# Kernel optimization log

Hardware: AMD Instinct MI355X
Metric: run time of the kernel (lower is better)

The kernel has to match this reference:

```python
import jax, jax.numpy as jnp
import numpy as np

B, T, D, H, V, NV = 64, 1024, 128, 256, 128, 3


def setup_inputs() -> dict:
    key = jax.random.key(0)
    ks = jax.random.split(key, 8)
    s_ih = 1.0 / np.sqrt(H)
    return {
        "x": jax.random.normal(ks[0], (B, T, D), dtype=jnp.float32),
        # PyTorch LSTM params: gate order i, f, g, o along the 4H axis
        "W_ih": jax.random.uniform(ks[1], (4 * H, D), minval=-s_ih, maxval=s_ih, dtype=jnp.float32),
        "W_hh": jax.random.uniform(ks[2], (4 * H, H), minval=-s_ih, maxval=s_ih, dtype=jnp.float32),
        "b_ih": jax.random.uniform(ks[3], (4 * H,), minval=-s_ih, maxval=s_ih, dtype=jnp.float32),
        "b_hh": jax.random.uniform(ks[4], (4 * H,), minval=-s_ih, maxval=s_ih, dtype=jnp.float32),
        "head_w": jax.random.uniform(ks[5], (NV, V, H), minval=-s_ih, maxval=s_ih, dtype=jnp.float32),
        "head_b": jax.random.uniform(ks[6], (NV, V), minval=-s_ih, maxval=s_ih, dtype=jnp.float32),
    }


def _lstm(x, W_ih, W_hh, b_ih, b_hh):
    Bc, Tc, _ = x.shape
    Hc = W_hh.shape[1]
    # Precompute input contribution for all timesteps in one GEMM: [B,T,4H]
    gx = jnp.einsum('btd,gd->btg', x, W_ih) + b_ih + b_hh
    gx = jnp.transpose(gx, (1, 0, 2))  # [T,B,4H] for scan over time

    def step(carry, g_t):
        h, c = carry
        g = g_t + h @ W_hh.T  # [B,4H]
        i, f, gg, o = jnp.split(g, 4, axis=-1)
        i = jax.nn.sigmoid(i)
        f = jax.nn.sigmoid(f)
        o = jax.nn.sigmoid(o)
        c = f * c + i * jnp.tanh(gg)
        h = o * jnp.tanh(c)
        return (h, c), h

    h0 = jnp.zeros((Bc, Hc), dtype=x.dtype)
    c0 = jnp.zeros((Bc, Hc), dtype=x.dtype)
    _, hs = jax.lax.scan(step, (h0, c0), gx)  # hs: [T,B,H]
    return jnp.transpose(hs, (1, 0, 2))  # [B,T,H]


def reference(x, W_ih, W_hh, b_ih, b_hh, head_w, head_b):
    out = _lstm(x, W_ih, W_hh, b_ih, b_hh)  # [B,T,H]
    # 3 parallel heads fused into one batched GEMM: [NV,B,T,V]
    logits = jnp.einsum('bth,nvh->nbtv', out, head_w) + head_b[:, None, None, :]
    return (logits[0], logits[1], logits[2])
```

## Files before the change

### kernel.cpp

```cpp
#include <hip/hip_runtime.h>
#include <hip/hip_bf16.h>
#include <math.h>

#define Bb 64
#define Tt 1024
#define Dd 128
#define Hh 256
#define G4 1024
#define Vv 128
#define NVh 3
#define BT (Bb*Tt)

typedef __fp16 half2_t __attribute__((ext_vector_type(2)));
typedef __fp16 f16x4 __attribute__((ext_vector_type(4)));
typedef __fp16 f16x8 __attribute__((ext_vector_type(8)));
typedef float f32x4 __attribute__((ext_vector_type(4)));

__device__ __forceinline__ half2_t pkh(float a, float b) {
    return __builtin_amdgcn_cvt_pkrtz(a, b);
}
__device__ __forceinline__ half2_t bch(unsigned int x) {
    return __builtin_bit_cast(half2_t, x);
}
__device__ __forceinline__ unsigned int bcu(half2_t x) {
    return __builtin_bit_cast(unsigned int, x);
}
__device__ __forceinline__ float fsig(float x) {
    return __builtin_amdgcn_rcpf(1.f + __expf(-x));
}
__device__ __forceinline__ float ftanh(float x) {
    float e = __expf(-2.f * fabsf(x));
    float r = (1.f - e) * __builtin_amdgcn_rcpf(1.f + e);
    return copysignf(r, x);
}
__device__ __forceinline__ f16x8 pk8f(const float* p) {
    float4 a = *(const float4*)p;
    float4 b = *(const float4*)(p + 4);
    uint4 u;
    u.x = bcu(pkh(a.x, a.y));
    u.y = bcu(pkh(a.z, a.w));
    u.z = bcu(pkh(b.x, b.y));
    u.w = bcu(pkh(b.z, b.w));
    return __builtin_bit_cast(f16x8, u);
}
__device__ __forceinline__ int sdot4(int a, int b, int c) {
#if __has_builtin(__builtin_amdgcn_sdot4)
    return __builtin_amdgcn_sdot4(a, b, c, false);
#else
    int r = c;
    #pragma unroll
    for (int i = 0; i < 4; ++i) {
        int av = (a << (24 - 8 * i)) >> 24;
        int bv = (b << (24 - 8 * i)) >> 24;
        r += av * bv;
    }
    return r;
#endif
}

__global__ __launch_bounds__(256) void cvt16(const float* __restrict__ in,
                                             __fp16* __restrict__ out, int n4) {
    int i = blockIdx.x * 256 + threadIdx.x;
    if (i < n4) {
        float4 v = ((const float4*)in)[i];
        f16x4 o;
        o[0] = (__fp16)v.x; o[1] = (__fp16)v.y;
        o[2] = (__fp16)v.z; o[3] = (__fp16)v.w;
        ((f16x4*)out)[i] = o;
    }
}

__global__ __launch_bounds__(256) void gx_mfma(const float* __restrict__ x,
                                               const __fp16* __restrict__ Wih16,
                                               const float* __restrict__ bih,
                                               const float* __restrict__ bhh,
                                               __fp16* __restrict__ gx2) {
    const int tid = threadIdx.x;
    const int w = tid >> 6, l = tid & 63;
    const int mb = blockIdx.x * 64 + w * 16;
    const int lr = l & 15, lk = l >> 4;

    f16x8 af[4];
    const float* xa = x + (size_t)(mb + lr) * Dd + lk * 8;
    #pragma unroll
    for (int ks = 0; ks < 4; ++ks) af[ks] = pk8f(xa + ks * 32);

    for (int jt = 0; jt < 16; ++jt) {
        f32x4 acc[4] = {};
        #pragma unroll
        for (int ks = 0; ks < 4; ++ks) {
            #pragma unroll
            for (int g = 0; g < 4; ++g) {
                const __fp16* bb = Wih16 + (size_t)(g * 256 + jt * 16 + lr) * Dd + ks * 32 + lk * 8;
                f16x8 bf = *(const f16x8*)bb;
                acc[g] = __builtin_amdgcn_mfma_f32_16x16x32_f16(af[ks], bf, acc[g], 0, 0, 0);
            }
        }
        float bsum[4];
        #pragma unroll
        for (int g = 0; g < 4; ++g) {
            int j = g * 256 + jt * 16 + lr;
            bsum[g] = bih[j] + bhh[j];
        }
        #pragma unroll
        for (int r = 0; r < 4; ++r) {
            int m = mb + lk * 4 + r;
            f16x4 o;
            o[0] = (__fp16)(acc[0][r] + bsum[0]);
            o[1] = (__fp16)(acc[1][r] + bsum[1]);
            o[2] = (__fp16)(acc[2][r] + bsum[2]);
            o[3] = (__fp16)(acc[3][r] + bsum[3]);
            *(f16x4*)&gx2[((size_t)m * Hh + jt * 16 + lr) * 4] = o;
        }
    }
}

__global__ __launch_bounds__(512, 2) void lstm_scan(const __fp16* __restrict__ gx2,
                                                    const float* __restrict__ Whh,
                                                    __fp16* __restrict__ hs16) {
    __shared__ __align__(16) unsigned int hq[64];
    __shared__ __align__(16) float4 pex[256];
    const int tid = threadIdx.x;
    const int jj = tid & 255;
    const int s = tid >> 8;
    const int b = blockIdx.x;

    int wq[4][32];
    #pragma unroll
    for (int g = 0; g < 4; ++g) {
        const float* wr = Whh + (size_t)(g * 256 + jj) * Hh + s * 128;
        #pragma unroll
        for (int c = 0; c < 32; ++c) {
            float4 f = *(const float4*)&wr[c * 4];
            int q0 = (int)rintf(f.x * 2032.f);
            int q1 = (int)rintf(f.y * 2032.f);
            int q2 = (int)rintf(f.z * 2032.f);
            int q3 = (int)rintf(f.w * 2032.f);
            wq[g][c] = (q0 & 255) | ((q1 & 255) << 8) | ((q2 & 255) << 16) | (q3 << 24);
        }
    }
    if (tid < 64) hq[tid] = 0u;
    float c_state = 0.f;
    __syncthreads();

    const __fp16* gxb = gx2 + ((size_t)b * Tt * Hh + jj) * 4;
    __fp16* hsb = hs16 + (size_t)b * Tt * Hh + jj;

    float g0 = 0.f, g1 = 0.f, g2 = 0.f, g3 = 0.f;
    if (s == 0) {
        uint2 gv = *(const uint2*)gxb;
        half2_t p = bch(gv.x), q = bch(gv.y);
        g0 = (float)p[0]; g1 = (float)p[1]; g2 = (float)q[0]; g3 = (float)q[1];
    }

    const uint4* h16 = (const uint4*)hq + (s << 3);
    __fp16 hprev = (__fp16)0.f;
    const float INV = 1.f / (2032.f * 127.f);

    for (int t = 0; t < Tt; ++t) {
        if (s == 0 && t > 0) hsb[(size_t)(t - 1) * Hh] = hprev;

        float n0 = 0.f, n1 = 0.f, n2 = 0.f, n3 = 0.f;
        if (s == 0) {
            const __fp16* gn = gxb + (size_t)(t + 1 < Tt ? t + 1 : t) * 1024;
            uint2 gv = *(const uint2*)gn;
            half2_t p = bch(gv.x), q = bch(gv.y);
            n0 = (float)p[0]; n1 = (float)p[1]; n2 = (float)q[0]; n3 = (float)q[1];
        }

        int a0 = 0, a1 = 0, a2 = 0, a3 = 0;
        #pragma unroll
        for (int q = 0; q < 8; ++q) {
            uint4 hv = h16[q];
            a0 = sdot4(wq[0][q*4+0], (int)hv.x, a0); a1 = sdot4(wq[1][q*4+0], (int)hv.x, a1);
            a2 = sdot4(wq[2][q*4+0], (int)hv.x, a2); a3 = sdot4(wq[3][q*4+0], (int)hv.x, a3);
            a0 = sdot4(wq[0][q*4+1], (int)hv.y, a0); a1 = sdot4(wq[1][q*4+1], (int)hv.y, a1);
            a2 = sdot4(wq[2][q*4+1], (int)hv.y, a2); a3 = sdot4(wq[3][q*4+1], (int)hv.y, a3);
            a0 = sdot4(wq[0][q*4+2], (int)hv.z, a0); a1 = sdot4(wq[1][q*4+2], (int)hv.z, a1);
            a2 = sdot4(wq[2][q*4+2], (int)hv.z, a2); a3 = sdot4(wq[3][q*4+2], (int)hv.z, a3);
            a0 = sdot4(wq[0][q*4+3], (int)hv.w, a0); a1 = sdot4(wq[1][q*4+3], (int)hv.w, a1);
            a2 = sdot4(wq[2][q*4+3], (int)hv.w, a2); a3 = sdot4(wq[3][q*4+3], (int)hv.w, a3);
        }

        if (s == 1) pex[jj] = make_float4((float)a0, (float)a1, (float)a2, (float)a3);
        __syncthreads();

        if (s == 0) {
            float4 pp = pex[jj];
            float A0 = ((float)a0 + pp.x) * INV + g0;
            float A1 = ((float)a1 + pp.y) * INV + g1;
            float A2 = ((float)a2 + pp.z) * INV + g2;
            float A3 = ((float)a3 + pp.w) * INV + g3;
            float si = fsig(A0);
            float sf = fsig(A1);
            float tg = ftanh(A2);
            float so = fsig(A3);
            c_state = sf * c_state + si * tg;
            float hn = so * ftanh(c_state);
            hprev = (__fp16)hn;
            ((signed char*)hq)[jj] = (signed char)(int)rintf(hn * 127.f);
        }
        g0 = n0; g1 = n1; g2 = n2; g3 = n3;
        __syncthreads();
    }
    if (s == 0) hsb[(size_t)(Tt - 1) * Hh] = hprev;
}

__global__ __launch_bounds__(256) void head_mfma(const __fp16* __restrict__ hs16,
                                                 const __fp16* __restrict__ hw16,
                                                 const float* __restrict__ hb,
                                                 float* __restrict__ out) {
    const int tid = threadIdx.x;
    const int w = tid >> 6, l = tid & 63;
    const int mb = blockIdx.x * 64 + w * 16;
    const int lr = l & 15, lk = l >> 4;

    f16x8 af[8];
    const __fp16* aa = hs16 + (size_t)(mb + lr) * Hh + lk * 8;
    #pragma unroll
    for (int ks = 0; ks < 8; ++ks) af[ks] = *(const f16x8*)(aa + ks * 32);

    for (int nt = 0; nt < 24; ++nt) {
        f32x4 acc = {};
        #pragma unroll
        for (int ks = 0; ks < 8; ++ks) {
            const __fp16* bb = hw16 + (size_t)(nt * 16 + lr) * Hh + ks * 32 + lk * 8;
            f16x8 bf = *(const f16x8*)bb;
            acc = __builtin_amdgcn_mfma_f32_16x16x32_f16(af[ks], bf, acc, 0, 0, 0);
        }
        int nv = nt * 16 + lr;
        int nh = nv >> 7, v = nv & 127;
        float bv = hb[nv];
        #pragma unroll
        for (int r = 0; r < 4; ++r) {
            int m = mb + lk * 4 + r;
            out[(size_t)nh * BT * Vv + (size_t)m * Vv + v] = acc[r] + bv;
        }
    }
}

extern "C" void kernel_launch(void* const* d_in, const int* in_sizes, int n_in,
                              void* d_out, int out_size, void* d_ws, size_t ws_size,
                              hipStream_t stream) {
    const float* x    = (const float*)d_in[0];
    const float* Wih  = (const float*)d_in[1];
    const float* Whh  = (const float*)d_in[2];
    const float* bih  = (const float*)d_in[3];
    const float* bhh  = (const float*)d_in[4];
    const float* hw   = (const float*)d_in[5];
    const float* hb   = (const float*)d_in[6];
    float* out = (float*)d_out;

    __fp16* Wih16 = (__fp16*)d_ws;
    __fp16* hw16  = Wih16 + (size_t)G4 * Dd;
    __fp16* gx2   = hw16 + (size_t)NVh * Vv * Hh;
    __fp16* hs16  = gx2 + (size_t)BT * G4;

    cvt16<<<(G4 * Dd / 4 + 255) / 256, 256, 0, stream>>>(Wih, Wih16, G4 * Dd / 4);
    cvt16<<<(NVh * Vv * Hh / 4 + 255) / 256, 256, 0, stream>>>(hw, hw16, NVh * Vv * Hh / 4);

    gx_mfma<<<BT / 64, 256, 0, stream>>>(x, Wih16, bih, bhh, gx2);
    lstm_scan<<<Bb, 512, 0, stream>>>(gx2, Whh, hs16);
    head_mfma<<<BT / 64, 256, 0, stream>>>(hs16, hw16, hb, out);
}
```

Before: 1.375 ms.

## Pair K-split lanes in a wave and double-buffer h to drop one barrier

The LSTM scan now places the two K-halves of each hidden unit in adjacent lanes of the same wave instead of separate thread halves. Partial dot products are combined with a lane shuffle, which removes the LDS exchange buffer. Double-buffering the quantized h vector then lets each timestep use one __syncthreads instead of two. In exchange, both lanes redundantly load gx and evaluate the gate nonlinearities.

```diff
diff --git a/kernel.cpp b/kernel.cpp
--- a/kernel.cpp
+++ b/kernel.cpp
@@ -118,11 +118,11 @@
 __global__ __launch_bounds__(512, 2) void lstm_scan(const __fp16* __restrict__ gx2,
                                                     const float* __restrict__ Whh,
                                                     __fp16* __restrict__ hs16) {
-    __shared__ __align__(16) unsigned int hq[64];
-    __shared__ __align__(16) float4 pex[256];
+    __shared__ __align__(16) unsigned int hq[2][64];
     const int tid = threadIdx.x;
-    const int jj = tid & 255;
-    const int s = tid >> 8;
+    const int w = tid >> 6, l = tid & 63;
+    const int s = l & 1;
+    const int jj = w * 32 + (l >> 1);
     const int b = blockIdx.x;
 
     int wq[4][32];
@@ -139,35 +139,36 @@
             wq[g][c] = (q0 & 255) | ((q1 & 255) << 8) | ((q2 & 255) << 16) | (q3 << 24);
         }
     }
-    if (tid < 64) hq[tid] = 0u;
+    if (tid < 128) ((unsigned int*)hq)[tid] = 0u;
     float c_state = 0.f;
     __syncthreads();
 
     const __fp16* gxb = gx2 + ((size_t)b * Tt * Hh + jj) * 4;
     __fp16* hsb = hs16 + (size_t)b * Tt * Hh + jj;
 
-    float g0 = 0.f, g1 = 0.f, g2 = 0.f, g3 = 0.f;
-    if (s == 0) {
+    float g0, g1, g2, g3;
+    {
         uint2 gv = *(const uint2*)gxb;
         half2_t p = bch(gv.x), q = bch(gv.y);
         g0 = (float)p[0]; g1 = (float)p[1]; g2 = (float)q[0]; g3 = (float)q[1];
     }
 
-    const uint4* h16 = (const uint4*)hq + (s << 3);
     __fp16 hprev = (__fp16)0.f;
     const float INV = 1.f / (2032.f * 127.f);
+    int cur = 0;
 
     for (int t = 0; t < Tt; ++t) {
         if (s == 0 && t > 0) hsb[(size_t)(t - 1) * Hh] = hprev;
 
-        float n0 = 0.f, n1 = 0.f, n2 = 0.f, n3 = 0.f;
-        if (s == 0) {
+        float n0, n1, n2, n3;
+        {
             const __fp16* gn = gxb + (size_t)(t + 1 < Tt ? t + 1 : t) * 1024;
             uint2 gv = *(const uint2*)gn;
             half2_t p = bch(gv.x), q = bch(gv.y);
             n0 = (float)p[0]; n1 = (float)p[1]; n2 = (float)q[0]; n3 = (float)q[1];
         }
 
+        const uint4* h16 = (const uint4*)hq[cur] + (s << 3);
         int a0 = 0, a1 = 0, a2 = 0, a3 = 0;
         #pragma unroll
         for (int q = 0; q < 8; ++q) {
@@ -182,26 +183,28 @@
             a2 = sdot4(wq[2][q*4+3], (int)hv.w, a2); a3 = sdot4(wq[3][q*4+3], (int)hv.w, a3);
         }
 
-        if (s == 1) pex[jj] = make_float4((float)a0, (float)a1, (float)a2, (float)a3);
-        __syncthreads();
-
-        if (s == 0) {
-            float4 pp = pex[jj];
-            float A0 = ((float)a0 + pp.x) * INV + g0;
-            float A1 = ((float)a1 + pp.y) * INV + g1;
-            float A2 = ((float)a2 + pp.z) * INV + g2;
-            float A3 = ((float)a3 + pp.w) * INV + g3;
-            float si = fsig(A0);
-            float sf = fsig(A1);
-            float tg = ftanh(A2);
-            float so = fsig(A3);
-            c_state = sf * c_state + si * tg;
-            float hn = so * ftanh(c_state);
-            hprev = (__fp16)hn;
-            ((signed char*)hq)[jj] = (signed char)(int)rintf(hn * 127.f);
-        }
+        a0 += __shfl_xor(a0, 1, 64);
+        a1 += __shfl_xor(a1, 1, 64);
+        a2 += __shfl_xor(a2, 1, 64);
+        a3 += __shfl_xor(a3, 1, 64);
+
+        float A0 = (float)a0 * INV + g0;
+        float A1 = (float)a1 * INV + g1;
+        float A2 = (float)a2 * INV + g2;
+        float A3 = (float)a3 * INV + g3;
+        float si = fsig(A0);
+        float sf = fsig(A1);
+        float tg = ftanh(A2);
+        float so = fsig(A3);
+        c_state = sf * c_state + si * tg;
+        float hn = so * ftanh(c_state);
+        hprev = (__fp16)hn;
+        if (s == 0)
+            ((signed char*)hq[cur ^ 1])[jj] = (signed char)(int)rintf(hn * 127.f);
+
         g0 = n0; g1 = n1; g2 = n2; g3 = n3;
         __syncthreads();
+        cur ^= 1;
     }
     if (s == 0) hsb[(size_t)(Tt - 1) * Hh] = hprev;
 }
```

New measurement: 1.199 ms. 1.15x faster.
